# Performance work log

Measured on AMD Instinct MI355X. Metric: run time of the kernel, lower is better.

Reference implementation:

```python
import jax, jax.numpy as jnp
import numpy as np

V = 32000; D = 128; L = 2048; B = 4
DI = 256; DS = 16; K = 4; H = 4; NM = 6; NA = 2; PAD = 0


def setup_inputs() -> dict:
    key = jax.random.key(0)
    ks = jax.random.split(key, 24)
    n = lambda i, shape, s: jax.random.normal(ks[i], shape, dtype=jnp.float32) * s
    inp = {}
    inp["input_ids"] = jax.random.randint(ks[0], (B, L), 0, V)
    inp["token_types"] = jax.random.randint(ks[1], (B, L), 0, 10)
    inp["timestamps"] = jax.random.uniform(ks[2], (B, L), dtype=jnp.float32)
    inp["emb"] = n(3, (V, D), 0.02).at[PAD].set(0.0)
    inp["type_emb"] = n(4, (10, D), 0.02)
    inp["te_freqs"] = n(5, (D // 2,), 0.1)
    inp["te_phases"] = jnp.zeros((D // 2,), jnp.float32)
    inp["te_w"] = n(6, (D, D), 0.05)
    inp["te_b"] = jnp.zeros((D,), jnp.float32)
    # Mamba blocks (stacked over NM)
    inp["m_norm_w"] = jnp.ones((NM, D), jnp.float32)
    inp["m_norm_b"] = jnp.zeros((NM, D), jnp.float32)
    inp["m_in_w"] = n(7, (NM, 2 * DI, D), 0.05)
    inp["m_conv_w"] = n(8, (NM, DI, 1, K), 0.2)   # depthwise, OIH with I=1
    inp["m_conv_b"] = jnp.zeros((NM, DI), jnp.float32)
    inp["m_dt_w"] = n(9, (NM, DI, DI), 0.05)
    inp["m_dt_b"] = jnp.zeros((NM, DI), jnp.float32)
    inp["m_B_w"] = n(10, (NM, DS, DI), 0.05)
    inp["m_C_w"] = n(11, (NM, DS, DI), 0.05)
    inp["m_D"] = jnp.ones((NM, DI), jnp.float32)
    inp["m_A_log"] = jnp.broadcast_to(jnp.log(jnp.arange(1, DS + 1, dtype=jnp.float32)), (NM, DI, DS)) + 0.0
    inp["m_out_w"] = n(12, (NM, D, DI), 0.05)
    # Attention blocks (stacked over NA)
    inp["a_ln1_w"] = jnp.ones((NA, D), jnp.float32)
    inp["a_ln1_b"] = jnp.zeros((NA, D), jnp.float32)
    inp["a_qkv_w"] = n(13, (NA, 3 * D, D), 0.05)
    inp["a_qkv_b"] = jnp.zeros((NA, 3 * D), jnp.float32)
    inp["a_out_w"] = n(14, (NA, D, D), 0.05)
    inp["a_out_b"] = jnp.zeros((NA, D), jnp.float32)
    inp["a_ln2_w"] = jnp.ones((NA, D), jnp.float32)
    inp["a_ln2_b"] = jnp.zeros((NA, D), jnp.float32)
    inp["a_f1_w"] = n(15, (NA, 4 * D, D), 0.05)
    inp["a_f1_b"] = jnp.zeros((NA, 4 * D), jnp.float32)
    inp["a_f2_w"] = n(16, (NA, D, 4 * D), 0.05)
    inp["a_f2_b"] = jnp.zeros((NA, D), jnp.float32)
    # Task head (n_tasks=1)
    inp["h_ln_w"] = jnp.ones((D,), jnp.float32)
    inp["h_ln_b"] = jnp.zeros((D,), jnp.float32)
    inp["h_w"] = n(17, (1, D), 0.05)
    inp["h_b"] = jnp.zeros((1,), jnp.float32)
    return inp


def _ln(x, w, b, eps=1e-5):
    mu = x.mean(-1, keepdims=True)
    var = ((x - mu) ** 2).mean(-1, keepdims=True)
    return (x - mu) * jax.lax.rsqrt(var + eps) * w + b


def _mamba(x, nw, nb, inw, cw, cb, dtw, dtb, bw, cpw, Dp, Alog, ow):
    res = x
    xn = _ln(x, nw, nb)
    xz = xn @ inw.T                              # [B,L,2*DI]
    xp, z = jnp.split(xz, 2, axis=-1)
    # causal depthwise conv: left-pad K-1, take first L outputs
    xc = jax.lax.conv_general_dilated(
        xp.transpose(0, 2, 1), cw, (1,), [(K - 1, 0)],
        feature_group_count=DI, dimension_numbers=("NCH", "OIH", "NCH"))
    xc = (xc + cb[None, :, None]).transpose(0, 2, 1)
    xc = jax.nn.silu(xc)
    dt = jax.nn.softplus(xc @ dtw.T + dtb)       # [B,L,DI]
    Bm = xc @ bw.T                               # [B,L,DS]
    Cm = xc @ cpw.T                              # [B,L,DS]
    A = -jnp.exp(Alog)                           # [DI,DS]

    def step(h, inp):
        dt_t, x_t, b_t, c_t = inp                # [B,DI],[B,DI],[B,DS],[B,DS]
        h = h * jnp.exp(A * dt_t[..., None]) + (x_t * dt_t)[..., None] * b_t[:, None, :]
        return h, (h * c_t[:, None, :]).sum(-1)

    xs = (jnp.moveaxis(dt, 1, 0), jnp.moveaxis(xc, 1, 0),
          jnp.moveaxis(Bm, 1, 0), jnp.moveaxis(Cm, 1, 0))
    h0 = jnp.zeros((x.shape[0], DI, DS), x.dtype)
    _, y = jax.lax.scan(step, h0, xs)            # y: [L,B,DI]
    y = jnp.moveaxis(y, 0, 1)
    y = y + xc * Dp
    y = y * jax.nn.silu(z)
    return res + y @ ow.T


def _attn(x, l1w, l1b, qkvw, qkvb, ow, ob, l2w, l2b, f1w, f1b, f2w, f2b):
    res = x
    xn = _ln(x, l1w, l1b)
    qkv = xn @ qkvw.T + qkvb
    q, k, v = jnp.split(qkv, 3, axis=-1)
    dh = D // H
    rs = lambda t: t.reshape(t.shape[0], t.shape[1], H, dh)
    q, k, v = rs(q), rs(k), rs(v)
    sc = jnp.einsum("bqhd,bkhd->bhqk", q, k) / jnp.sqrt(jnp.float32(dh))
    p = jax.nn.softmax(sc, axis=-1)
    o = jnp.einsum("bhqk,bkhd->bqhd", p, v).reshape(x.shape)
    x = res + o @ ow.T + ob
    ff = jax.nn.gelu(_ln(x, l2w, l2b) @ f1w.T + f1b, approximate=False) @ f2w.T + f2b
    return x + ff


def reference(input_ids, token_types, timestamps, emb, type_emb, te_freqs, te_phases, te_w, te_b,
              m_norm_w, m_norm_b, m_in_w, m_conv_w, m_conv_b, m_dt_w, m_dt_b, m_B_w, m_C_w,
              m_D, m_A_log, m_out_w,
              a_ln1_w, a_ln1_b, a_qkv_w, a_qkv_b, a_out_w, a_out_b, a_ln2_w, a_ln2_b,
              a_f1_w, a_f1_b, a_f2_w, a_f2_b, h_ln_w, h_ln_b, h_w, h_b):
    t = timestamps[..., None]
    enc = jnp.concatenate([jnp.sin(t * te_freqs + te_phases),
                           jnp.cos(t * te_freqs + te_phases)], axis=-1)
    x = emb[input_ids] + type_emb[token_types] + enc @ te_w.T + te_b
    attn_every = (NM + NA) // NA
    mi = 0; ai = 0
    for i in range(NM + NA):
        if (i + 1) % attn_every == 0:
            x = _attn(x, a_ln1_w[ai], a_ln1_b[ai], a_qkv_w[ai], a_qkv_b[ai],
                      a_out_w[ai], a_out_b[ai], a_ln2_w[ai], a_ln2_b[ai],
                      a_f1_w[ai], a_f1_b[ai], a_f2_w[ai], a_f2_b[ai])
            ai += 1
        else:
            x = _mamba(x, m_norm_w[mi], m_norm_b[mi], m_in_w[mi], m_conv_w[mi], m_conv_b[mi],
                       m_dt_w[mi], m_dt_b[mi], m_B_w[mi], m_C_w[mi], m_D[mi], m_A_log[mi], m_out_w[mi])
            mi += 1
    cls = x[:, 0, :]
    return (_ln(cls, h_ln_w, h_ln_b) @ h_w.T + h_b)[:, 0]
```

## Files before the change

kernel.cpp:

```cpp
#include <hip/hip_runtime.h>
#include <hip/hip_bf16.h>
#include <math.h>

constexpr int Ll = 2048, Bb = 4, DIi = 256, Hh = 4;
constexpr int TOK = Bb * Ll;
constexpr int NC = 128;
constexpr int CH = 16;
constexpr float LOG2E = 1.442695040888963f;

#define DEV __device__ __forceinline__

DEV float siluf(float v)     { return v / (1.f + expf(-v)); }
DEV float softplusf(float v) { return (v > 20.f) ? v : log1pf(expf(v)); }
DEV float geluf(float v)     { return 0.5f * v * (1.f + erff(v * 0.7071067811865476f)); }

#if defined(__has_builtin)
#if __has_builtin(__builtin_amdgcn_exp2f)
#define EXP2F __builtin_amdgcn_exp2f
#endif
#endif
#ifndef EXP2F
#define EXP2F exp2f
#endif

DEV short f2bf(float f) {
    union { float f; unsigned u; } a; a.f = f;
    unsigned r = (a.u + 0x7fffu + ((a.u >> 16) & 1u)) >> 16;
    return (short)r;
}

using bf16x8 = __attribute__((ext_vector_type(8))) short;
using f16x8  = __attribute__((ext_vector_type(8))) _Float16;
using f32x4  = __attribute__((ext_vector_type(4))) float;

__global__ __launch_bounds__(256) void wprep_kernel(
    const float* s0, const float* s1, const float* s2, const float* s3,
    const float* s4, const float* s5, const float* s6, const float* s7,
    const float* s8, const float* s9, _Float16* dst)
{
    constexpr int base[10] = {0, 16384, 409600, 802816, 827392, 851968,
                              1048576, 1146880, 1179648, 1310720};
    constexpr int nseg[10] = {16384, 393216, 393216, 24576, 24576, 196608,
                              98304, 32768, 131072, 131072};
    int seg = blockIdx.y;
    int t = blockIdx.x * 256 + threadIdx.x;
    if (t >= nseg[seg]) return;
    const float* src;
    switch (seg) {
        case 0: src = s0; break; case 1: src = s1; break;
        case 2: src = s2; break; case 3: src = s3; break;
        case 4: src = s4; break; case 5: src = s5; break;
        case 6: src = s6; break; case 7: src = s7; break;
        case 8: src = s8; break; default: src = s9; break;
    }
    dst[base[seg] + t] = (_Float16)src[t];
}

__global__ __launch_bounds__(256) void gather_enc_kernel(
    const int* __restrict__ ids, const int* __restrict__ tts,
    const float* __restrict__ ts, const float* __restrict__ emb,
    const float* __restrict__ temb, const float* __restrict__ freqs,
    const float* __restrict__ phases, float* __restrict__ x,
    float* __restrict__ enc)
{
    int tok = blockIdx.x * 2 + (threadIdx.x >> 7);
    int d = threadIdx.x & 127;
    float tval = ts[tok];
    int j = d & 63;
    float a = tval * freqs[j] + phases[j];
    enc[(size_t)tok * 128 + d] = (d < 64) ? sinf(a) : cosf(a);
    int id = ids[tok];
    int tt = tts[tok];
    x[(size_t)tok * 128 + d] = emb[(size_t)id * 128 + d] + temb[(size_t)tt * 128 + d];
}

template <int ACT, bool BIAS, bool ADD, bool LNA, int MODE, bool STATS>
__global__ __launch_bounds__(256) void gemm64_kernel(
    const float* __restrict__ A, const _Float16* __restrict__ W,
    const float* __restrict__ bias, float* __restrict__ C,
    const float* __restrict__ lnw, const float* __restrict__ lnb,
    float* __restrict__ statsbuf,
    const _Float16* __restrict__ Bw, const _Float16* __restrict__ Cw,
    float* __restrict__ bmo, float* __restrict__ cmo,
    short* __restrict__ kbf, short* __restrict__ vbf,
    int M, int N, int Kd, int lda, int ldc)
{
    __shared__ _Float16 As[64][72];
    __shared__ _Float16 Ws[64][72];
    __shared__ float sRow[STATS ? 2 : 1][STATS ? 64 : 1][2];
    const int by = blockIdx.y;
    const bool isBC = (MODE == 1) && (by == (int)gridDim.y - 1);
    const int bm0 = blockIdx.x * 64, bn0 = by * 64;
    const int tid = threadIdx.x;
    const int w = tid >> 6, l = tid & 63;
    const int wr = w >> 1, wc = w & 1;
    const int fr = l & 15, fk = (l >> 4) * 8;
    const int srow = tid >> 2, skc = (tid & 3) * 16;
    float mu = 0.f, rstd = 1.f;
    if (LNA) {
        float4 st = *(const float4*)(statsbuf + (size_t)(bm0 + srow) * 4);
        mu = (st.x + st.z) * (1.f / 128.f);
        float var = (st.y + st.w) * (1.f / 128.f) - mu * mu;
        rstd = rsqrtf(var + 1e-5f);
    }
    f32x4 acc[2][2] = {};

    for (int k0 = 0; k0 < Kd; k0 += 64) {
        const float* ap = A + (size_t)(bm0 + srow) * lda + k0 + skc;
        const _Float16* wp;
        if (isBC) {
            if (srow < 16)      wp = Bw + (size_t)srow * Kd + k0 + skc;
            else if (srow < 32) wp = Cw + (size_t)(srow - 16) * Kd + k0 + skc;
            else                wp = Bw + k0 + skc;
        } else {
            wp = W + (size_t)(bn0 + srow) * Kd + k0 + skc;
        }
        float af[16];
#pragma unroll
        for (int q = 0; q < 4; q++)
            *(float4*)(af + q * 4) = *(const float4*)(ap + q * 4);
        f16x8 wb0 = *(const f16x8*)wp;
        f16x8 wb1 = *(const f16x8*)(wp + 8);
        if (LNA) {
#pragma unroll
            for (int q = 0; q < 4; q++) {
                float4 w4 = *(const float4*)(lnw + k0 + skc + q * 4);
                float4 b4 = *(const float4*)(lnb + k0 + skc + q * 4);
                af[q*4+0] = (af[q*4+0] - mu) * rstd * w4.x + b4.x;
                af[q*4+1] = (af[q*4+1] - mu) * rstd * w4.y + b4.y;
                af[q*4+2] = (af[q*4+2] - mu) * rstd * w4.z + b4.z;
                af[q*4+3] = (af[q*4+3] - mu) * rstd * w4.w + b4.w;
            }
        }
        f16x8 ab0, ab1;
#pragma unroll
        for (int q = 0; q < 8; q++) {
            ab0[q] = (_Float16)af[q]; ab1[q] = (_Float16)af[q + 8];
        }
        __syncthreads();
        *(f16x8*)&As[srow][skc]     = ab0;
        *(f16x8*)&As[srow][skc + 8] = ab1;
        *(f16x8*)&Ws[srow][skc]     = wb0;
        *(f16x8*)&Ws[srow][skc + 8] = wb1;
        __syncthreads();
#pragma unroll
        for (int ks = 0; ks < 64; ks += 32) {
            f16x8 afr0 = *(const f16x8*)&As[wr * 32 + fr][ks + fk];
            f16x8 afr1 = *(const f16x8*)&As[wr * 32 + 16 + fr][ks + fk];
            f16x8 wfr0 = *(const f16x8*)&Ws[wc * 32 + fr][ks + fk];
            f16x8 wfr1 = *(const f16x8*)&Ws[wc * 32 + 16 + fr][ks + fk];
            acc[0][0] = __builtin_amdgcn_mfma_f32_16x16x32_f16(afr0, wfr0, acc[0][0], 0, 0, 0);
            acc[0][1] = __builtin_amdgcn_mfma_f32_16x16x32_f16(afr0, wfr1, acc[0][1], 0, 0, 0);
            acc[1][0] = __builtin_amdgcn_mfma_f32_16x16x32_f16(afr1, wfr0, acc[1][0], 0, 0, 0);
            acc[1][1] = __builtin_amdgcn_mfma_f32_16x16x32_f16(afr1, wfr1, acc[1][1], 0, 0, 0);
        }
    }
    float rs_[2][4], rq_[2][4];
    if (STATS) {
#pragma unroll
        for (int ri = 0; ri < 2; ri++)
#pragma unroll
            for (int r = 0; r < 4; r++) { rs_[ri][r] = 0.f; rq_[ri][r] = 0.f; }
    }
#pragma unroll
    for (int ri = 0; ri < 2; ri++)
#pragma unroll
    for (int ci = 0; ci < 2; ci++) {
        const int lcol = wc * 32 + ci * 16 + fr;
        const int col = bn0 + lcol;
        const int row0 = bm0 + wr * 32 + ri * 16 + (l >> 4) * 4;
        if (isBC) {
            if (lcol < 32) {
                float* dst = (lcol < 16) ? bmo : cmo;
                const int cc = lcol & 15;
#pragma unroll
                for (int r = 0; r < 4; r++)
                    dst[(size_t)(row0 + r) * 16 + cc] = acc[ri][ci][r];
            }
        } else if (MODE == 2) {
            const float bv = bias[col];
            const int b = row0 >> 11, tl0 = row0 & 2047;
            if (col < 128) {
#pragma unroll
                for (int r = 0; r < 4; r++)
                    C[(size_t)(row0 + r) * 128 + col] = acc[ri][ci][r] + bv;
            } else if (col < 256) {
                const int hc = col - 128;
                short* kp = kbf + ((size_t)(b * 4 + (hc >> 5)) * 2048 + tl0) * 32 + (hc & 31);
#pragma unroll
                for (int r = 0; r < 4; r++)
                    kp[(size_t)r * 32] = f2bf(acc[ri][ci][r] + bv);
            } else {
                const int hc = col - 256;
                short4 vk;
#pragma unroll
                for (int r = 0; r < 4; r++)
                    ((short*)&vk)[r] = f2bf(acc[ri][ci][r] + bv);
                *(short4*)(vbf + ((size_t)(b * 4 + (hc >> 5)) * 32 + (hc & 31)) * 2048 + tl0) = vk;
            }
        } else {
            const float bv = BIAS ? bias[col] : 0.f;
#pragma unroll
            for (int r = 0; r < 4; r++) {
                float t = acc[ri][ci][r] + bv;
                if (ACT == 1) t = softplusf(t);
                if (ACT == 2) t = geluf(t);
                float* p = C + (size_t)(row0 + r) * ldc + col;
                if (ADD) t += *p;
                *p = t;
                if (STATS) { rs_[ri][r] += t; rq_[ri][r] += t * t; }
            }
        }
    }
    if (STATS) {
        const int g = l >> 4;
#pragma unroll
        for (int ri = 0; ri < 2; ri++)
#pragma unroll
        for (int r = 0; r < 4; r++) {
            float v = rs_[ri][r], q = rq_[ri][r];
            v += __shfl_xor(v, 1); q += __shfl_xor(q, 1);
            v += __shfl_xor(v, 2); q += __shfl_xor(q, 2);
            v += __shfl_xor(v, 4); q += __shfl_xor(q, 4);
            v += __shfl_xor(v, 8); q += __shfl_xor(q, 8);
            if (fr == 0) {
                int rowl = wr * 32 + ri * 16 + g * 4 + r;
                sRow[wc][rowl][0] = v;
                sRow[wc][rowl][1] = q;
            }
        }
        __syncthreads();
        if (tid < 128) {
            int row = tid >> 1, j = tid & 1;
            statsbuf[(size_t)(bm0 + row) * 4 + by * 2 + j] =
                sRow[0][row][j] + sRow[1][row][j];
        }
    }
}

__global__ __launch_bounds__(256) void conv_kernel(
    const float* __restrict__ xz, const float* __restrict__ cw,
    const float* __restrict__ cb, float* __restrict__ xc)
{
    int g = blockIdx.x * 256 + threadIdx.x;
    int c4 = g & 63;
    int t  = (g >> 6) & 2047;
    int b  = g >> 17;
    int c  = c4 * 4;
    float4 w0 = *(const float4*)(cw + (size_t)c * 4);
    float4 w1 = *(const float4*)(cw + (size_t)(c + 1) * 4);
    float4 w2 = *(const float4*)(cw + (size_t)(c + 2) * 4);
    float4 w3 = *(const float4*)(cw + (size_t)(c + 3) * 4);
    float4 bi = *(const float4*)(cb + c);
    float4 xk[4];
#pragma unroll
    for (int kk = 0; kk < 4; kk++) {
        int tt = t - 3 + kk;
        if (tt >= 0) xk[kk] = *(const float4*)(xz + ((size_t)b * 2048 + tt) * 512 + c);
        else xk[kk] = make_float4(0.f, 0.f, 0.f, 0.f);
    }
    float4 r;
    r.x = bi.x + xk[0].x * w0.x + xk[1].x * w0.y + xk[2].x * w0.z + xk[3].x * w0.w;
    r.y = bi.y + xk[0].y * w1.x + xk[1].y * w1.y + xk[2].y * w1.z + xk[3].y * w1.w;
    r.z = bi.z + xk[0].z * w2.x + xk[1].z * w2.y + xk[2].z * w2.z + xk[3].z * w2.w;
    r.w = bi.w + xk[0].w * w3.x + xk[1].w * w3.y + xk[2].w * w3.z + xk[3].w * w3.w;
    r.x = siluf(r.x); r.y = siluf(r.y); r.z = siluf(r.z); r.w = siluf(r.w);
    *(float4*)(xc + ((size_t)b * 2048 + t) * 256 + c) = r;
}

__global__ __launch_bounds__(256) void scan1_kernel(
    const float* __restrict__ dt, const float* __restrict__ xc,
    const float* __restrict__ bm, const float* __restrict__ Alog,
    float* __restrict__ F, float* __restrict__ sumdt)
{
    int c = threadIdx.x;
    int k = blockIdx.x & (NC - 1);
    int b = blockIdx.x / NC;
    __shared__ float sB[CH][16];
    int t0 = k * CH;
    if (threadIdx.x < CH * 4) {
        int r = threadIdx.x >> 2, c4 = (threadIdx.x & 3) << 2;
        *(float4*)&sB[r][c4] = *(const float4*)(bm + ((size_t)b * 2048 + t0 + r) * 16 + c4);
    }
    float A2[16];
#pragma unroll
    for (int s = 0; s < 16; s++) A2[s] = -expf(Alog[(size_t)c * 16 + s]) * LOG2E;
    __syncthreads();
    float h[16] = {};
    float sd = 0.f;
    size_t base = ((size_t)b * 2048 + t0) * 256 + c;
    for (int tt = 0; tt < CH; tt++) {
        float d  = dt[base + (size_t)tt * 256];
        float xv = xc[base + (size_t)tt * 256];
        sd += d;
        float xdt = xv * d;
#pragma unroll
        for (int s = 0; s < 16; s++) h[s] = h[s] * EXP2F(A2[s] * d) + xdt * sB[tt][s];
    }
    size_t fo = (((size_t)b * NC + k) * 256 + c) * 16;
#pragma unroll
    for (int s = 0; s < 16; s += 4) *(float4*)(F + fo + s) = make_float4(h[s], h[s+1], h[s+2], h[s+3]);
    sumdt[((size_t)b * NC + k) * 256 + c] = sd;
}

__global__ __launch_bounds__(256) void scan2_kernel(
    float* __restrict__ F, const float* __restrict__ sumdt,
    const float* __restrict__ Alog)
{
    int g = blockIdx.x * 256 + threadIdx.x;
    int s = g & 15, c = (g >> 4) & 255, b = g >> 12;
    float A2 = -expf(Alog[(size_t)c * 16 + s]) * LOG2E;
    float h = 0.f;
    for (int k = 0; k < NC; k++) {
        size_t o = (((size_t)b * NC + k) * 256 + c) * 16 + s;
        float tmp = F[o];
        F[o] = h;
        h = h * EXP2F(A2 * sumdt[((size_t)b * NC + k) * 256 + c]) + tmp;
    }
}

__global__ __launch_bounds__(256) void scan3_kernel(
    const float* __restrict__ dt, const float* __restrict__ xc,
    const float* __restrict__ bm, const float* __restrict__ cm,
    const float* __restrict__ xz, const float* __restrict__ Alog,
    const float* __restrict__ Dp, const float* __restrict__ Hs,
    float* __restrict__ y)
{
    int c = threadIdx.x;
    int k = blockIdx.x & (NC - 1);
    int b = blockIdx.x / NC;
    __shared__ float sB[CH][16], sC[CH][16];
    int t0 = k * CH;
    if (threadIdx.x < CH * 4) {
        int r = threadIdx.x >> 2, c4 = (threadIdx.x & 3) << 2;
        *(float4*)&sB[r][c4] = *(const float4*)(bm + ((size_t)b * 2048 + t0 + r) * 16 + c4);
        *(float4*)&sC[r][c4] = *(const float4*)(cm + ((size_t)b * 2048 + t0 + r) * 16 + c4);
    }
    float A2[16];
#pragma unroll
    for (int s = 0; s < 16; s++) A2[s] = -expf(Alog[(size_t)c * 16 + s]) * LOG2E;
    __syncthreads();
    float h[16];
    size_t ho = (((size_t)b * NC + k) * 256 + c) * 16;
#pragma unroll
    for (int s = 0; s < 16; s++) h[s] = Hs[ho + s];
    float Dv = Dp[c];
    size_t base  = ((size_t)b * 2048 + t0) * 256 + c;
    size_t zbase = ((size_t)b * 2048 + t0) * 512 + 256 + c;
    for (int tt = 0; tt < CH; tt++) {
        float d  = dt[base + (size_t)tt * 256];
        float xv = xc[base + (size_t)tt * 256];
        float xdt = xv * d;
        float yv = 0.f;
#pragma unroll
        for (int s = 0; s < 16; s++) {
            h[s] = h[s] * EXP2F(A2[s] * d) + xdt * sB[tt][s];
            yv += h[s] * sC[tt][s];
        }
        yv += xv * Dv;
        float zv = xz[zbase + (size_t)tt * 512];
        y[base + (size_t)tt * 256] = yv * siluf(zv);
    }
}

__global__ __launch_bounds__(256) void attn_part_kernel(
    const float* __restrict__ qbuf, const short* __restrict__ kbf,
    const short* __restrict__ vbf, float* __restrict__ pO, float* __restrict__ pml)
{
    __shared__ short Klds[2][64 * 32];
    __shared__ short Vlds[2][32 * 64];
    __shared__ short Pt[4][64][18];
    const int qt = blockIdx.x, b = blockIdx.z;
    const int h = blockIdx.y >> 2, sp = blockIdx.y & 3;
    const int tid = threadIdx.x;
    const int w = tid >> 6, l = tid & 63;
    const int q16 = l & 15, g = l >> 4;
    const float cQ = 0.25503634043f;

    const int qrow = qt * 64 + w * 16 + q16;
    const float* qp = qbuf + ((size_t)(b * 2048 + qrow)) * 128 + 32 * h + g * 8;
    bf16x8 qfrag;
    {
        float qf[8];
        *(float4*)qf       = *(const float4*)qp;
        *(float4*)(qf + 4) = *(const float4*)(qp + 4);
#pragma unroll
        for (int i = 0; i < 8; i++) qfrag[i] = f2bf(qf[i] * cQ);
    }
    const int bh = b * 4 + h;
    const short* kb = kbf + ((size_t)bh * 2048) * 32;
    const short* vb = vbf + ((size_t)bh * 32) * 2048;

    const int vrow = tid >> 3;
    const int vsw  = ((tid & 7) * 16) ^ ((vrow & 7) << 4);
    const int ts0 = sp * 8;

    bf16x8 kst, vst;
    auto ldregs = [&](int t) {
        kst = *(const bf16x8*)(kb + (size_t)t * 2048 + tid * 8);
        vst = *(const bf16x8*)(vb + (size_t)vrow * 2048 + t * 64 + (vsw >> 1));
    };
    auto dswrite = [&](int buf) {
        *(bf16x8*)&Klds[buf][tid * 8] = kst;
        *(bf16x8*)&Vlds[buf][tid * 8] = vst;
    };

    float m = -1e30f, lsum = 0.f;
    f32x4 O0 = {0.f, 0.f, 0.f, 0.f}, O1 = {0.f, 0.f, 0.f, 0.f};
    const f32x4 zf = {0.f, 0.f, 0.f, 0.f};

    auto step = [&](int buf) {
        bf16x8 kf[4];
#pragma unroll
        for (int kt = 0; kt < 4; kt++)
            kf[kt] = *(const bf16x8*)&Klds[buf][(kt * 16 + q16) * 32 + g * 8];
        f32x4 St[4];
#pragma unroll
        for (int kt = 0; kt < 4; kt++)
            St[kt] = __builtin_amdgcn_mfma_f32_16x16x32_bf16(kf[kt], qfrag, zf, 0, 0, 0);
        float pm = St[0][0];
#pragma unroll
        for (int kt = 0; kt < 4; kt++)
#pragma unroll
            for (int r = 0; r < 4; r++) pm = fmaxf(pm, St[kt][r]);
        pm = fmaxf(pm, __shfl_xor(pm, 16));
        pm = fmaxf(pm, __shfl_xor(pm, 32));
        float mn = fmaxf(m, pm);
        float rs = EXP2F(m - mn);
        float ps = 0.f;
#pragma unroll
        for (int kt = 0; kt < 4; kt++)
#pragma unroll
            for (int r = 0; r < 4; r++) {
                float p = EXP2F(St[kt][r] - mn);
                ps += p;
                Pt[w][kt * 16 + g * 4 + r][q16] = f2bf(p);
            }
        ps += __shfl_xor(ps, 16);
        ps += __shfl_xor(ps, 32);
        lsum = lsum * rs + ps;
        m = mn;
        O0 *= rs; O1 *= rs;
#pragma unroll
        for (int c = 0; c < 2; c++) {
            bf16x8 pb;
#pragma unroll
            for (int i = 0; i < 8; i++) pb[i] = Pt[w][c * 32 + g * 8 + i][q16];
#pragma unroll
            for (int hf = 0; hf < 2; hf++) {
                const int d = q16 + 16 * hf;
                bf16x8 vf = *(const bf16x8*)&Vlds[buf][d * 64 + ((c * 32 + g * 8) ^ ((d & 7) << 3))];
                if (hf == 0) O0 = __builtin_amdgcn_mfma_f32_16x16x32_bf16(vf, pb, O0, 0, 0, 0);
                else         O1 = __builtin_amdgcn_mfma_f32_16x16x32_bf16(vf, pb, O1, 0, 0, 0);
            }
        }
    };

    ldregs(ts0);
    dswrite(0);
    ldregs(ts0 + 1);
    int cur = 0;
    for (int i = 0; i < 8; i++) {
        __syncthreads();
        if (i + 1 < 8) {
            dswrite(cur ^ 1);
            if (i + 2 < 8) ldregs(ts0 + i + 2);
        }
        step(cur);
        cur ^= 1;
    }

    size_t po = (((size_t)(bh * 4 + sp)) * 2048 + qrow) * 32;
#pragma unroll
    for (int r = 0; r < 4; r++) {
        pO[po + g * 4 + r]      = O0[r];
        pO[po + 16 + g * 4 + r] = O1[r];
    }
    if (g == 0) {
        size_t mo = (((size_t)(bh * 4 + sp)) * 2048 + qrow) * 2;
        pml[mo]     = m;
        pml[mo + 1] = lsum;
    }
}

__global__ __launch_bounds__(256) void attn_comb_kernel(
    const float* __restrict__ pO, const float* __restrict__ pml,
    float* __restrict__ aout)
{
    int gid = blockIdx.x * 256 + threadIdx.x;
    int d = gid & 31, q = (gid >> 5) & 2047, bh = gid >> 16;
    float m[4], lv[4], M = -1e30f;
#pragma unroll
    for (int s = 0; s < 4; s++) {
        size_t mo = (((size_t)(bh * 4 + s)) * 2048 + q) * 2;
        m[s] = pml[mo]; lv[s] = pml[mo + 1];
        M = fmaxf(M, m[s]);
    }
    float L = 0.f, o = 0.f;
#pragma unroll
    for (int s = 0; s < 4; s++) {
        float wgt = EXP2F(m[s] - M);
        L += lv[s] * wgt;
        o += pO[(((size_t)(bh * 4 + s)) * 2048 + q) * 32 + d] * wgt;
    }
    int b = bh >> 2, h = bh & 3;
    aout[((size_t)(b * 2048 + q)) * 128 + h * 32 + d] = o / L;
}

__global__ __launch_bounds__(128) void head_kernel(
    const float* __restrict__ x, const float* __restrict__ w,
    const float* __restrict__ bsp, const float* __restrict__ hw,
    const float* __restrict__ hb, float* __restrict__ out)
{
    int bb = blockIdx.x;
    int d = threadIdx.x;
    int wid = d >> 6, lane = d & 63;
    float v = x[(size_t)bb * 2048 * 128 + d];
    float s = v, sq = v * v;
#pragma unroll
    for (int o = 32; o > 0; o >>= 1) { s += __shfl_xor(s, o); sq += __shfl_xor(sq, o); }
    __shared__ float red[4];
    if (lane == 0) { red[wid] = s; red[2 + wid] = sq; }
    __syncthreads();
    s = red[0] + red[1]; sq = red[2] + red[3];
    float mu = s * (1.f / 128.f);
    float var = sq * (1.f / 128.f) - mu * mu;
    float xn = (v - mu) * rsqrtf(var + 1e-5f) * w[d] + bsp[d];
    float pr = xn * hw[d];
#pragma unroll
    for (int o = 32; o > 0; o >>= 1) pr += __shfl_xor(pr, o);
    __syncthreads();
    if (lane == 0) red[wid] = pr;
    __syncthreads();
    if (d == 0) out[bb] = red[0] + red[1] + hb[0];
}

constexpr size_t OFF_X  = 0;
constexpr size_t OFF_XZ = (size_t)1 << 20;
constexpr size_t OFF_XC = (size_t)5 << 20;
constexpr size_t OFF_DT = (size_t)7 << 20;
constexpr size_t OFF_Y  = (size_t)9 << 20;
constexpr size_t OFF_BM = (size_t)11 << 20;
constexpr size_t OFF_CM = OFF_BM + 131072;
constexpr size_t OFF_SD = OFF_CM + 131072;
constexpr size_t OFF_ST = OFF_SD + 131072;
constexpr size_t OFF_F  = OFF_ST + 32768;
constexpr size_t OFF_WF = OFF_F + ((size_t)2 << 20);
constexpr size_t WS_FLOATS = OFF_WF + 720896;

extern "C" void kernel_launch(void* const* d_in, const int* in_sizes, int n_in,
                              void* d_out, int out_size, void* d_ws, size_t ws_size,
                              hipStream_t stream)
{
    const int*   ids   = (const int*)d_in[0];
    const int*   tts   = (const int*)d_in[1];
    const float* tstmp = (const float*)d_in[2];
    const float* emb   = (const float*)d_in[3];
    const float* temb  = (const float*)d_in[4];
    const float* tef   = (const float*)d_in[5];
    const float* tep   = (const float*)d_in[6];
    const float* tew   = (const float*)d_in[7];
    const float* tebi  = (const float*)d_in[8];
    const float* mnw   = (const float*)d_in[9];
    const float* mnb   = (const float*)d_in[10];
    const float* minw  = (const float*)d_in[11];
    const float* mcwp  = (const float*)d_in[12];
    const float* mcb   = (const float*)d_in[13];
    const float* mdtw  = (const float*)d_in[14];
    const float* mdtb  = (const float*)d_in[15];
    const float* mbw   = (const float*)d_in[16];
    const float* mcw2  = (const float*)d_in[17];
    const float* mD    = (const float*)d_in[18];
    const float* mAl   = (const float*)d_in[19];
    const float* mow   = (const float*)d_in[20];
    const float* al1w  = (const float*)d_in[21];
    const float* al1b  = (const float*)d_in[22];
    const float* aqkvw = (const float*)d_in[23];
    const float* aqkvb = (const float*)d_in[24];
    const float* aow   = (const float*)d_in[25];
    const float* aob   = (const float*)d_in[26];
    const float* al2w  = (const float*)d_in[27];
    const float* al2b  = (const float*)d_in[28];
    const float* af1w  = (const float*)d_in[29];
    const float* af1b  = (const float*)d_in[30];
    const float* af2w  = (const float*)d_in[31];
    const float* af2b  = (const float*)d_in[32];
    const float* hlnw  = (const float*)d_in[33];
    const float* hlnb  = (const float*)d_in[34];
    const float* hw    = (const float*)d_in[35];
    const float* hb    = (const float*)d_in[36];
    float* out = (float*)d_out;
    float* wsf = (float*)d_ws;
    if (ws_size < WS_FLOATS * sizeof(float)) return;

    float* x    = wsf + OFF_X;
    float* xz   = wsf + OFF_XZ;
    float* xc   = wsf + OFF_XC;
    float* dtb  = wsf + OFF_DT;
    float* yb   = wsf + OFF_Y;
    float* bm   = wsf + OFF_BM;
    float* cm   = wsf + OFF_CM;
    float* sdb  = wsf + OFF_SD;
    float* stats4 = wsf + OFF_ST;
    float* Fb   = wsf + OFF_F;
    float* ff   = xz;
    float* aout = yb;
    float* qbuf = xc;
    float* pO   = xz;
    float* pml  = dtb;
    float* encb = Fb;
    short* kbf  = (short*)(wsf + OFF_F);
    short* vbf  = (short*)(wsf + OFF_F + ((size_t)1 << 20));
    _Float16* wf16 = (_Float16*)(wsf + OFF_WF);

    const _Float16* tew16   = wf16;
    const _Float16* minw16  = wf16 + 16384;
    const _Float16* mdtw16  = wf16 + 409600;
    const _Float16* mbw16   = wf16 + 802816;
    const _Float16* mcw216  = wf16 + 827392;
    const _Float16* mow16   = wf16 + 851968;
    const _Float16* aqkvw16 = wf16 + 1048576;
    const _Float16* aow16   = wf16 + 1146880;
    const _Float16* af1w16  = wf16 + 1179648;
    const _Float16* af2w16  = wf16 + 1310720;

    wprep_kernel<<<dim3(1536, 10), 256, 0, stream>>>(
        tew, minw, mdtw, mbw, mcw2, mow, aqkvw, aow, af1w, af2w, wf16);

    gather_enc_kernel<<<TOK / 2, 256, 0, stream>>>(ids, tts, tstmp, emb, temb, tef, tep, x, encb);
    gemm64_kernel<0, true, true, false, 0, true><<<dim3(128, 2), 256, 0, stream>>>(
        encb, tew16, tebi, x, nullptr, nullptr, stats4, nullptr, nullptr,
        nullptr, nullptr, nullptr, nullptr, TOK, 128, 128, 128, 128);

    int mi = 0, ai = 0;
    for (int i = 0; i < 8; i++) {
        if ((i + 1) % 4 == 0) {
            gemm64_kernel<0, true, false, true, 2, false><<<dim3(128, 6), 256, 0, stream>>>(
                x, aqkvw16 + (size_t)ai * 49152, aqkvb + ai * 384, qbuf,
                al1w + ai * 128, al1b + ai * 128, stats4, nullptr, nullptr,
                nullptr, nullptr, kbf, vbf, TOK, 384, 128, 128, 128);
            attn_part_kernel<<<dim3(32, 16, Bb), 256, 0, stream>>>(qbuf, kbf, vbf, pO, pml);
            attn_comb_kernel<<<4096, 256, 0, stream>>>(pO, pml, aout);
            gemm64_kernel<0, true, true, false, 0, true><<<dim3(128, 2), 256, 0, stream>>>(
                aout, aow16 + (size_t)ai * 16384, aob + ai * 128, x,
                nullptr, nullptr, stats4, nullptr, nullptr,
                nullptr, nullptr, nullptr, nullptr, TOK, 128, 128, 128, 128);
            gemm64_kernel<2, true, false, true, 0, false><<<dim3(128, 8), 256, 0, stream>>>(
                x, af1w16 + (size_t)ai * 65536, af1b + ai * 512, ff,
                al2w + ai * 128, al2b + ai * 128, stats4, nullptr, nullptr,
                nullptr, nullptr, nullptr, nullptr, TOK, 512, 128, 128, 512);
            gemm64_kernel<0, true, true, false, 0, true><<<dim3(128, 2), 256, 0, stream>>>(
                ff, af2w16 + (size_t)ai * 65536, af2b + ai * 128, x,
                nullptr, nullptr, stats4, nullptr, nullptr,
                nullptr, nullptr, nullptr, nullptr, TOK, 128, 512, 512, 128);
            ai++;
        } else {
            const float* Al = mAl + (size_t)mi * DIi * 16;
            gemm64_kernel<0, false, false, true, 0, false><<<dim3(128, 8), 256, 0, stream>>>(
                x, minw16 + (size_t)mi * 65536, nullptr, xz,
                mnw + mi * 128, mnb + mi * 128, stats4, nullptr, nullptr,
                nullptr, nullptr, nullptr, nullptr, TOK, 512, 128, 128, 512);
            conv_kernel<<<2048, 256, 0, stream>>>(xz, mcwp + (size_t)mi * DIi * 4, mcb + mi * DIi, xc);
            gemm64_kernel<1, true, false, false, 1, false><<<dim3(128, 5), 256, 0, stream>>>(
                xc, mdtw16 + (size_t)mi * 65536, mdtb + mi * 256, dtb,
                nullptr, nullptr, nullptr,
                mbw16 + (size_t)mi * 4096, mcw216 + (size_t)mi * 4096,
                bm, cm, nullptr, nullptr, TOK, 256, 256, 256, 256);
            scan1_kernel<<<Bb * NC, 256, 0, stream>>>(dtb, xc, bm, Al, Fb, sdb);
            scan2_kernel<<<64, 256, 0, stream>>>(Fb, sdb, Al);
            scan3_kernel<<<Bb * NC, 256, 0, stream>>>(dtb, xc, bm, cm, xz, Al, mD + mi * 256, Fb, yb);
            gemm64_kernel<0, false, true, false, 0, true><<<dim3(128, 2), 256, 0, stream>>>(
                yb, mow16 + (size_t)mi * 32768, nullptr, x,
                nullptr, nullptr, stats4, nullptr, nullptr,
                nullptr, nullptr, nullptr, nullptr, TOK, 128, 256, 256, 128);
            mi++;
        }
    }
    head_kernel<<<Bb, 128, 0, stream>>>(x, hlnw, hlnb, hw, hb, out);
}
```

Before: 661.4 us.

## Fuse three-phase chunked scan into one cooperative kernel with grid syncs

Replaces the three separate scan launches (chunk-local scan, cross-chunk prefix, chunk re-scan with output) with a single cooperative kernel that uses grid-wide syncs between phases. Each block keeps its A coefficients and shared B/C tiles across phases, and the launch overhead and kernel boundaries of two extra launches go away. The trade-offs are the cost of the grid barriers, idle blocks during the serial middle phase (only 64 of 512 blocks work), and a requirement that all 512 blocks be co-resident for the cooperative launch to succeed.

Measured after the change: 1.423 ms. 2.15x slower.

```diff
diff --git a/kernel.cpp b/kernel.cpp
--- a/kernel.cpp
+++ b/kernel.cpp
@@ -1,6 +1,9 @@
 #include <hip/hip_runtime.h>
 #include <hip/hip_bf16.h>
+#include <hip/hip_cooperative_groups.h>
 #include <math.h>
+
+namespace cg = cooperative_groups;
 
 constexpr int Ll = 2048, Bb = 4, DIi = 256, Hh = 4;
 constexpr int TOK = Bb * Ll;
@@ -268,27 +271,32 @@
     *(float4*)(xc + ((size_t)b * 2048 + t) * 256 + c) = r;
 }
 
-__global__ __launch_bounds__(256) void scan1_kernel(
+__global__ __launch_bounds__(256) void scan_fused_kernel(
     const float* __restrict__ dt, const float* __restrict__ xc,
-    const float* __restrict__ bm, const float* __restrict__ Alog,
-    float* __restrict__ F, float* __restrict__ sumdt)
-{
-    int c = threadIdx.x;
-    int k = blockIdx.x & (NC - 1);
-    int b = blockIdx.x / NC;
-    __shared__ float sB[CH][16];
-    int t0 = k * CH;
+    const float* __restrict__ bm, const float* __restrict__ cm,
+    const float* __restrict__ xz, const float* __restrict__ Alog,
+    const float* __restrict__ Dp, float* __restrict__ F,
+    float* __restrict__ sumdt, float* __restrict__ y)
+{
+    cg::grid_group grid = cg::this_grid();
+    const int c = threadIdx.x;
+    const int k = blockIdx.x & (NC - 1);
+    const int b = blockIdx.x / NC;
+    __shared__ float sB[CH][16], sC[CH][16];
+    const int t0 = k * CH;
     if (threadIdx.x < CH * 4) {
         int r = threadIdx.x >> 2, c4 = (threadIdx.x & 3) << 2;
         *(float4*)&sB[r][c4] = *(const float4*)(bm + ((size_t)b * 2048 + t0 + r) * 16 + c4);
+        *(float4*)&sC[r][c4] = *(const float4*)(cm + ((size_t)b * 2048 + t0 + r) * 16 + c4);
     }
     float A2[16];
 #pragma unroll
     for (int s = 0; s < 16; s++) A2[s] = -expf(Alog[(size_t)c * 16 + s]) * LOG2E;
     __syncthreads();
+
     float h[16] = {};
     float sd = 0.f;
-    size_t base = ((size_t)b * 2048 + t0) * 256 + c;
+    const size_t base = ((size_t)b * 2048 + t0) * 256 + c;
     for (int tt = 0; tt < CH; tt++) {
         float d  = dt[base + (size_t)tt * 256];
         float xv = xc[base + (size_t)tt * 256];
@@ -297,56 +305,32 @@
 #pragma unroll
         for (int s = 0; s < 16; s++) h[s] = h[s] * EXP2F(A2[s] * d) + xdt * sB[tt][s];
     }
-    size_t fo = (((size_t)b * NC + k) * 256 + c) * 16;
+    const size_t fo = (((size_t)b * NC + k) * 256 + c) * 16;
 #pragma unroll
     for (int s = 0; s < 16; s += 4) *(float4*)(F + fo + s) = make_float4(h[s], h[s+1], h[s+2], h[s+3]);
     sumdt[((size_t)b * NC + k) * 256 + c] = sd;
-}
-
-__global__ __launch_bounds__(256) void scan2_kernel(
-    float* __restrict__ F, const float* __restrict__ sumdt,
-    const float* __restrict__ Alog)
-{
-    int g = blockIdx.x * 256 + threadIdx.x;
-    int s = g & 15, c = (g >> 4) & 255, b = g >> 12;
-    float A2 = -expf(Alog[(size_t)c * 16 + s]) * LOG2E;
-    float h = 0.f;
-    for (int k = 0; k < NC; k++) {
-        size_t o = (((size_t)b * NC + k) * 256 + c) * 16 + s;
-        float tmp = F[o];
-        F[o] = h;
-        h = h * EXP2F(A2 * sumdt[((size_t)b * NC + k) * 256 + c]) + tmp;
-    }
-}
-
-__global__ __launch_bounds__(256) void scan3_kernel(
-    const float* __restrict__ dt, const float* __restrict__ xc,
-    const float* __restrict__ bm, const float* __restrict__ cm,
-    const float* __restrict__ xz, const float* __restrict__ Alog,
-    const float* __restrict__ Dp, const float* __restrict__ Hs,
-    float* __restrict__ y)
-{
-    int c = threadIdx.x;
-    int k = blockIdx.x & (NC - 1);
-    int b = blockIdx.x / NC;
-    __shared__ float sB[CH][16], sC[CH][16];
-    int t0 = k * CH;
-    if (threadIdx.x < CH * 4) {
-        int r = threadIdx.x >> 2, c4 = (threadIdx.x & 3) << 2;
-        *(float4*)&sB[r][c4] = *(const float4*)(bm + ((size_t)b * 2048 + t0 + r) * 16 + c4);
-        *(float4*)&sC[r][c4] = *(const float4*)(cm + ((size_t)b * 2048 + t0 + r) * 16 + c4);
-    }
-    float A2[16];
-#pragma unroll
-    for (int s = 0; s < 16; s++) A2[s] = -expf(Alog[(size_t)c * 16 + s]) * LOG2E;
-    __syncthreads();
-    float h[16];
-    size_t ho = (((size_t)b * NC + k) * 256 + c) * 16;
-#pragma unroll
-    for (int s = 0; s < 16; s++) h[s] = Hs[ho + s];
+
+    grid.sync();
+
+    if (blockIdx.x < 64) {
+        int g = blockIdx.x * 256 + threadIdx.x;
+        int s2 = g & 15, c2 = (g >> 4) & 255, b2 = g >> 12;
+        float A2p = -expf(Alog[(size_t)c2 * 16 + s2]) * LOG2E;
+        float hp = 0.f;
+        for (int kk = 0; kk < NC; kk++) {
+            size_t o = (((size_t)b2 * NC + kk) * 256 + c2) * 16 + s2;
+            float tmp = F[o];
+            F[o] = hp;
+            hp = hp * EXP2F(A2p * sumdt[((size_t)b2 * NC + kk) * 256 + c2]) + tmp;
+        }
+    }
+
+    grid.sync();
+
+#pragma unroll
+    for (int s = 0; s < 16; s++) h[s] = F[fo + s];
     float Dv = Dp[c];
-    size_t base  = ((size_t)b * 2048 + t0) * 256 + c;
-    size_t zbase = ((size_t)b * 2048 + t0) * 512 + 256 + c;
+    const size_t zbase = ((size_t)b * 2048 + t0) * 512 + 256 + c;
     for (int tt = 0; tt < CH; tt++) {
         float d  = dt[base + (size_t)tt * 256];
         float xv = xc[base + (size_t)tt * 256];
@@ -656,6 +640,7 @@
             ai++;
         } else {
             const float* Al = mAl + (size_t)mi * DIi * 16;
+            const float* Dpv = mD + (size_t)mi * 256;
             gemm64_kernel<0, false, false, true, 0, false><<<dim3(128, 8), 256, 0, stream>>>(
                 x, minw16 + (size_t)mi * 65536, nullptr, xz,
                 mnw + mi * 128, mnb + mi * 128, stats4, nullptr, nullptr,
@@ -666,9 +651,13 @@
                 nullptr, nullptr, nullptr,
                 mbw16 + (size_t)mi * 4096, mcw216 + (size_t)mi * 4096,
                 bm, cm, nullptr, nullptr, TOK, 256, 256, 256, 256);
-            scan1_kernel<<<Bb * NC, 256, 0, stream>>>(dtb, xc, bm, Al, Fb, sdb);
-            scan2_kernel<<<64, 256, 0, stream>>>(Fb, sdb, Al);
-            scan3_kernel<<<Bb * NC, 256, 0, stream>>>(dtb, xc, bm, cm, xz, Al, mD + mi * 256, Fb, yb);
+            {
+                void* scanArgs[10] = {
+                    (void*)&dtb, (void*)&xc, (void*)&bm, (void*)&cm, (void*)&xz,
+                    (void*)&Al, (void*)&Dpv, (void*)&Fb, (void*)&sdb, (void*)&yb };
+                hipLaunchCooperativeKernel((const void*)scan_fused_kernel,
+                                           dim3(Bb * NC), dim3(256), scanArgs, 0, stream);
+            }
             gemm64_kernel<0, false, true, false, 0, true><<<dim3(128, 2), 256, 0, stream>>>(
                 yb, mow16 + (size_t)mi * 32768, nullptr, x,
                 nullptr, nullptr, stats4, nullptr, nullptr,
```
